# Kernel optimization log

Hardware: AMD Instinct MI355X
Metric: run time of the kernel (lower is better)

The kernel has to match this reference:

```python
import jax, jax.numpy as jnp
import numpy as np

B, D, S, L = 4, 512, 2048, 8921

def setup_inputs() -> dict:
    key = jax.random.key(0)
    ks = jax.random.split(key, 4)
    H = jax.random.normal(ks[0], (B, D, S), dtype=jnp.float32)
    # 1x1 conv weights collapse to [out, in] matrices (xavier-ish scale)
    Wk = jax.random.normal(ks[1], (D, D), dtype=jnp.float32) * (1.0 / np.sqrt(D))
    Wv = jax.random.normal(ks[2], (D, D), dtype=jnp.float32) * (1.0 / np.sqrt(D))
    bk = jnp.full((D,), 0.01, dtype=jnp.float32)
    bv = jnp.full((D,), 0.01, dtype=jnp.float32)
    Q = jax.random.normal(ks[3], (L, D), dtype=jnp.float32) * 0.02
    return {"H": H, "Wk": Wk, "bk": bk, "Wv": Wv, "bv": bv, "Q": Q}

def reference(H, Wk, bk, Wv, bv, Q):
    # K/V: 1x1 Conv1d over channels + bias, ELU, permute(0,2,1) -> [B,S,D]
    K = jax.nn.elu(jnp.einsum('od,bds->bso', Wk, H) + bk)
    V = jax.nn.elu(jnp.einsum('od,bds->bso', Wv, H) + bv)
    # TargetAttention: energy E = Q K^T -> [B,L,S], softmax over seq (scale=False)
    E = jnp.einsum('ld,bsd->bls', Q, K)
    A = jax.nn.softmax(E, axis=-1)
    C = jnp.einsum('bls,bsd->bld', A, V)  # [B, L, D]
    return (C, A)
```

## Files before the change

### kernel.cpp

```cpp
#include <hip/hip_runtime.h>
#include <math.h>

#define Bn 4
#define Dn 512
#define Sn 2048
#define Ln 8921
#define Lpad 8960

typedef short bf16x8 __attribute__((ext_vector_type(8)));
typedef float f32x4 __attribute__((ext_vector_type(4)));

__device__ __forceinline__ float elu1(float x) {
    return x > 0.f ? x : expm1f(x);
}

__device__ __forceinline__ unsigned f2bf(float f) {
    unsigned u = __float_as_uint(f);
    u += 0x7FFFu + ((u >> 16) & 1u);
    return u >> 16;
}
__device__ __forceinline__ unsigned pack2(float a, float b) {
    return f2bf(a) | (f2bf(b) << 16);
}
__device__ __forceinline__ unsigned pack_bf_trunc(float lo, float hi) {
    return __builtin_amdgcn_perm(__float_as_uint(hi), __float_as_uint(lo), 0x07060302u);
}
__device__ __forceinline__ void gld_lds16(const void* g, void* l) {
    __builtin_amdgcn_global_load_lds((const __attribute__((address_space(1))) int*)g,
                                     (__attribute__((address_space(3))) int*)l, 16, 0, 0);
}

__global__ __launch_bounds__(256) void h_transpose(const float* __restrict__ H,
                                                   short* __restrict__ Ht) {
    int b = blockIdx.z;
    int s0 = blockIdx.x * 64, d0 = blockIdx.y * 64;
    __shared__ float tile[64][65];
    int t = threadIdx.x;
    int r = t >> 4, c4 = (t & 15) * 4;
    const float* Hb = H + (size_t)b * Dn * Sn;
#pragma unroll
    for (int i = 0; i < 4; ++i) {
        float4 v = *(const float4*)(Hb + (size_t)(d0 + i * 16 + r) * Sn + s0 + c4);
        *(float4*)&tile[i * 16 + r][c4] = v;
    }
    __syncthreads();
#pragma unroll
    for (int i = 0; i < 4; ++i) {
        int srow = i * 16 + r;
        float v0 = tile[c4 + 0][srow], v1 = tile[c4 + 1][srow];
        float v2 = tile[c4 + 2][srow], v3 = tile[c4 + 3][srow];
        uint2 o = make_uint2(pack2(v0, v1), pack2(v2, v3));
        *(uint2*)(Ht + ((size_t)b * Sn + s0 + srow) * Dn + d0 + c4) = o;
    }
}

__global__ __launch_bounds__(256) void f32_to_bf16(const float* __restrict__ src,
                                                   short* __restrict__ dst, int n8) {
    int id = blockIdx.x * 256 + threadIdx.x;
    if (id >= n8) return;
    const float* s = src + (size_t)id * 8;
    float4 a = *(const float4*)s;
    float4 b = *(const float4*)(s + 4);
    uint4 o = {pack2(a.x, a.y), pack2(a.z, a.w), pack2(b.x, b.y), pack2(b.z, b.w)};
    *(uint4*)(dst + (size_t)id * 8) = o;
}

__global__ __launch_bounds__(256) void q_to_bf16(const float* __restrict__ Q,
                                                 short* __restrict__ Qb) {
    int id = blockIdx.x * 256 + threadIdx.x;
    int row = id >> 6, c = (id & 63) * 8;
    uint4 o = {0, 0, 0, 0};
    if (row < Ln) {
        const float* src = Q + (size_t)row * Dn + c;
        float4 a = *(const float4*)src;
        float4 b = *(const float4*)(src + 4);
        o.x = pack2(a.x, a.y); o.y = pack2(a.z, a.w);
        o.z = pack2(b.x, b.y); o.w = pack2(b.z, b.w);
    }
    *(uint4*)(Qb + (size_t)id * 8) = o;
}

template <int OUT_BF16, int EPI>
__global__ __launch_bounds__(256) void gemm_nt(const short* __restrict__ A,
                                               const short* __restrict__ B,
                                               const float* __restrict__ bias,
                                               void* __restrict__ Out,
                                               int K, int lda, int ldb, int ldo,
                                               int mmax,
                                               long bA, long bB, long bO) {
    const int b  = blockIdx.z;
    const int n0 = blockIdx.x * 128;
    const int m0 = blockIdx.y * 128;
    __shared__ short lA[128 * 32];
    __shared__ short lB[128 * 32];
    const int t = threadIdx.x;
    const int lane = t & 63, w = t >> 6;
    const int wm = (w & 1) * 64, wn = (w >> 1) * 64;
    const int quad = lane >> 4, l15 = lane & 15;
    f32x4 acc[4][4] = {};
    const short* Ab = A + (size_t)bA * b + (size_t)m0 * lda;
    const short* Bb = B + (size_t)bB * b + (size_t)n0 * ldb;
    const int sr = t >> 2, ss = (t & 3) * 8;

    for (int k0 = 0; k0 < K; k0 += 32) {
        gld_lds16(Ab + (size_t)sr * lda + k0 + ss,        lA + t * 8);
        gld_lds16(Ab + (size_t)(sr + 64) * lda + k0 + ss, lA + 2048 + t * 8);
        gld_lds16(Bb + (size_t)sr * ldb + k0 + ss,        lB + t * 8);
        gld_lds16(Bb + (size_t)(sr + 64) * ldb + k0 + ss, lB + 2048 + t * 8);
        __syncthreads();
        bf16x8 af[4], bfr[4];
#pragma unroll
        for (int i = 0; i < 4; ++i)
            af[i] = *(const bf16x8*)&lA[(wm + i * 16 + l15) * 32 + quad * 8];
#pragma unroll
        for (int j = 0; j < 4; ++j)
            bfr[j] = *(const bf16x8*)&lB[(wn + j * 16 + l15) * 32 + quad * 8];
#pragma unroll
        for (int i = 0; i < 4; ++i)
#pragma unroll
            for (int j = 0; j < 4; ++j)
                acc[i][j] = __builtin_amdgcn_mfma_f32_16x16x32_bf16(af[i], bfr[j], acc[i][j], 0, 0, 0);
        __syncthreads();
    }

#pragma unroll
    for (int i = 0; i < 4; ++i) {
        int mb = m0 + wm + i * 16 + quad * 4;
#pragma unroll
        for (int r = 0; r < 4; ++r) {
            int m = mb + r;
            if (m < mmax) {
                float bm = (EPI == 2) ? bias[m] : 0.f;
#pragma unroll
                for (int j = 0; j < 4; ++j) {
                    int col = n0 + wn + j * 16 + l15;
                    float v = acc[i][j][r];
                    if (EPI == 1) v = elu1(v + bias[col]);
                    if (EPI == 2) v = elu1(v + bm);
                    if (OUT_BF16)
                        ((short*)Out)[(size_t)bO * b + (size_t)m * ldo + col] = (short)f2bf(v);
                    else
                        ((float*)Out)[(size_t)bO * b + (size_t)m * ldo + col] = v;
                }
            }
        }
    }
}

template <int OUT_BF16>
__global__ __launch_bounds__(512, 2) void gemm_nt256(const short* __restrict__ A,
                                                     const short* __restrict__ B,
                                                     void* __restrict__ Out,
                                                     int K, int lda, int ldb, int ldo,
                                                     int mmax,
                                                     long bA, long bB, long bO) {
    const int b  = blockIdx.z;
    const int n0 = blockIdx.x * 256;
    const int m0 = blockIdx.y * 256;
    __shared__ short lds[65536];
    const int t = threadIdx.x;
    const int lane = t & 63, w = t >> 6;
    const int wm = w >> 2, wn = w & 3;
    const int quad = lane >> 4, l15 = lane & 15;
    const int xr = (l15 >> 1) & 3;

    const short* Ab = A + (size_t)bA * b + (size_t)m0 * lda;
    const short* Bb = B + (size_t)bB * b + (size_t)n0 * ldb;

    const short* srcA[2]; const short* srcB[2];
    int dstA[2], dstB[2];
#pragma unroll
    for (int i = 0; i < 2; ++i) {
        int p = i * 512 + t;
        int g = p ^ ((p >> 3) & 3);
        int row = g >> 2, q = g & 3;
        srcA[i] = Ab + (size_t)row * lda + q * 8;
        srcB[i] = Bb + (size_t)row * ldb + q * 8;
        dstA[i] = p * 8;
        dstB[i] = 8192 + p * 8;
    }

    int offA[8], offB[4];
#pragma unroll
    for (int m = 0; m < 8; ++m) {
        int c = (wm * 128 + m * 16 + l15) * 4 + quad;
        offA[m] = (c ^ xr) * 8;
    }
#pragma unroll
    for (int j = 0; j < 4; ++j) {
        int c = (wn * 64 + j * 16 + l15) * 4 + quad;
        offB[j] = 8192 + (c ^ xr) * 8;
    }

    f32x4 acc[8][4] = {};
    const int NK = K >> 5;

    auto STAGE = [&](int kt) {
        const int slot = (kt & 3) * 16384;
        const int ko = kt * 32;
#pragma unroll
        for (int i = 0; i < 2; ++i) {
            gld_lds16(srcA[i] + ko, &lds[slot + dstA[i]]);
            gld_lds16(srcB[i] + ko, &lds[slot + dstB[i]]);
        }
    };

    STAGE(0); STAGE(1); STAGE(2);

    for (int k = 0; k < NK; ++k) {
        asm volatile("s_waitcnt lgkmcnt(0)" ::: "memory");
        if (k < NK - 2)
            asm volatile("s_waitcnt vmcnt(8)" ::: "memory");
        else if (k == NK - 2)
            asm volatile("s_waitcnt vmcnt(4)" ::: "memory");
        else
            asm volatile("s_waitcnt vmcnt(0)" ::: "memory");
        __builtin_amdgcn_s_barrier();
        asm volatile("" ::: "memory");
        if (k + 3 < NK) STAGE(k + 3);
        const short* sl = &lds[(k & 3) * 16384];
        bf16x8 af[8], bfv[4];
#pragma unroll
        for (int m = 0; m < 8; ++m) af[m] = *(const bf16x8*)(sl + offA[m]);
#pragma unroll
        for (int j = 0; j < 4; ++j) bfv[j] = *(const bf16x8*)(sl + offB[j]);
#pragma unroll
        for (int m = 0; m < 8; ++m)
#pragma unroll
            for (int j = 0; j < 4; ++j)
                acc[m][j] = __builtin_amdgcn_mfma_f32_16x16x32_bf16(af[m], bfv[j], acc[m][j], 0, 0, 0);
    }

#pragma unroll
    for (int m = 0; m < 8; ++m) {
        int mb = m0 + wm * 128 + m * 16 + quad * 4;
#pragma unroll
        for (int r = 0; r < 4; ++r) {
            int mm = mb + r;
            if (mm < mmax) {
#pragma unroll
                for (int j = 0; j < 4; ++j) {
                    int col = n0 + wn * 64 + j * 16 + l15;
                    float v = acc[m][j][r];
                    if (OUT_BF16)
                        ((short*)Out)[(size_t)bO * b + (size_t)mm * ldo + col] = (short)f2bf(v);
                    else
                        ((float*)Out)[(size_t)bO * b + (size_t)mm * ldo + col] = v;
                }
            }
        }
    }
}

__global__ __launch_bounds__(256) void softmax_bf16(short* __restrict__ EA,
                                                    float* __restrict__ Aout) {
    int row = blockIdx.x;
    int b = row / Ln, l = row - b * Ln;
    short* pe = EA + ((size_t)b * Lpad + l) * Sn;
    float* pa = Aout + (size_t)row * Sn;
    int t = threadIdx.x;
    uint4 raw = *(const uint4*)(pe + t * 8);
    unsigned pw[4] = {raw.x, raw.y, raw.z, raw.w};
    float v[8];
#pragma unroll
    for (int q = 0; q < 4; ++q) {
        v[2 * q]     = __uint_as_float(pw[q] << 16);
        v[2 * q + 1] = __uint_as_float(pw[q] & 0xFFFF0000u);
    }
    float m = v[0];
#pragma unroll
    for (int i = 1; i < 8; ++i) m = fmaxf(m, v[i]);
#pragma unroll
    for (int off = 32; off >= 1; off >>= 1) m = fmaxf(m, __shfl_xor(m, off));
    __shared__ float sm[4], ssum[4];
    int lane = t & 63, wv = t >> 6;
    if (lane == 0) sm[wv] = m;
    __syncthreads();
    m = fmaxf(fmaxf(sm[0], sm[1]), fmaxf(sm[2], sm[3]));
    float s = 0.f;
#pragma unroll
    for (int i = 0; i < 8; ++i) {
        v[i] = expf(v[i] - m);
        s += v[i];
    }
#pragma unroll
    for (int off = 32; off >= 1; off >>= 1) s += __shfl_xor(s, off);
    if (lane == 0) ssum[wv] = s;
    __syncthreads();
    s = ssum[0] + ssum[1] + ssum[2] + ssum[3];
    float inv = 1.f / s;
#pragma unroll
    for (int i = 0; i < 8; ++i) v[i] *= inv;
    float4 o0 = {v[0], v[1], v[2], v[3]};
    float4 o1 = {v[4], v[5], v[6], v[7]};
    *(float4*)(pa + t * 8)     = o0;
    *(float4*)(pa + t * 8 + 4) = o1;
    uint4 ob = {pack2(v[0], v[1]), pack2(v[2], v[3]), pack2(v[4], v[5]), pack2(v[6], v[7])};
    *(uint4*)(pe + t * 8) = ob;
}

__global__ __launch_bounds__(256) void softmax_f32(float* __restrict__ E) {
    size_t row = blockIdx.x;
    float* p = E + row * (size_t)Sn;
    int t = threadIdx.x;
    float4 u0 = *(const float4*)(p + t * 8);
    float4 u1 = *(const float4*)(p + t * 8 + 4);
    float v[8] = {u0.x, u0.y, u0.z, u0.w, u1.x, u1.y, u1.z, u1.w};
    float m = v[0];
#pragma unroll
    for (int i = 1; i < 8; ++i) m = fmaxf(m, v[i]);
#pragma unroll
    for (int off = 32; off >= 1; off >>= 1) m = fmaxf(m, __shfl_xor(m, off));
    __shared__ float sm[4], ssum[4];
    int lane = t & 63, wv = t >> 6;
    if (lane == 0) sm[wv] = m;
    __syncthreads();
    m = fmaxf(fmaxf(sm[0], sm[1]), fmaxf(sm[2], sm[3]));
    float s = 0.f;
#pragma unroll
    for (int i = 0; i < 8; ++i) {
        v[i] = expf(v[i] - m);
        s += v[i];
    }
#pragma unroll
    for (int off = 32; off >= 1; off >>= 1) s += __shfl_xor(s, off);
    if (lane == 0) ssum[wv] = s;
    __syncthreads();
    s = ssum[0] + ssum[1] + ssum[2] + ssum[3];
    float inv = 1.f / s;
#pragma unroll
    for (int i = 0; i < 8; ++i) v[i] *= inv;
    float4 o0 = {v[0], v[1], v[2], v[3]};
    float4 o1 = {v[4], v[5], v[6], v[7]};
    *(float4*)(p + t * 8)     = o0;
    *(float4*)(p + t * 8 + 4) = o1;
}

__global__ __launch_bounds__(256) void c_mfma_f32(const float* __restrict__ A,
                                                  const short* __restrict__ Vt,
                                                  float* __restrict__ C) {
    const int b  = blockIdx.z;
    const int n0 = blockIdx.x * 128;
    const int m0 = blockIdx.y * 128;
    __shared__ short lA[128 * 32];
    __shared__ short lB[128 * 32];
    const int t = threadIdx.x;
    const int lane = t & 63, w = t >> 6;
    const int wm = (w & 1) * 64, wn = (w >> 1) * 64;
    const int quad = lane >> 4, l15 = lane & 15;
    f32x4 acc[4][4] = {};
    const float* Ab = A + (size_t)b * Ln * Sn;
    const short* Bb = Vt + (size_t)b * Dn * Sn + (size_t)n0 * Sn;
    const int ar = t >> 1, ah = (t & 1) * 16;
    const int br = t >> 2, bs = (t & 3) * 8;
    const int am = m0 + ar;
    const bool arow_ok = (am < Ln);
    const float* asrc0 = Ab + (size_t)am * Sn + ah;

    for (int s0 = 0; s0 < Sn; s0 += 32) {
        gld_lds16(Bb + (size_t)br * Sn + s0 + bs,        lB + t * 8);
        gld_lds16(Bb + (size_t)(br + 64) * Sn + s0 + bs, lB + 2048 + t * 8);
        unsigned p[8] = {0, 0, 0, 0, 0, 0, 0, 0};
        if (arow_ok) {
            const float* src = asrc0 + s0;
            float4 f0 = *(const float4*)(src);
            float4 f1 = *(const float4*)(src + 4);
            float4 f2 = *(const float4*)(src + 8);
            float4 f3 = *(const float4*)(src + 12);
            p[0] = pack_bf_trunc(f0.x, f0.y); p[1] = pack_bf_trunc(f0.z, f0.w);
            p[2] = pack_bf_trunc(f1.x, f1.y); p[3] = pack_bf_trunc(f1.z, f1.w);
            p[4] = pack_bf_trunc(f2.x, f2.y); p[5] = pack_bf_trunc(f2.z, f2.w);
            p[6] = pack_bf_trunc(f3.x, f3.y); p[7] = pack_bf_trunc(f3.z, f3.w);
        }
        *(uint4*)&lA[ar * 32 + ah]     = *(uint4*)&p[0];
        *(uint4*)&lA[ar * 32 + ah + 8] = *(uint4*)&p[4];
        __syncthreads();
        bf16x8 af[4], bfr[4];
#pragma unroll
        for (int i = 0; i < 4; ++i)
            af[i] = *(const bf16x8*)&lA[(wm + i * 16 + l15) * 32 + quad * 8];
#pragma unroll
        for (int j = 0; j < 4; ++j)
            bfr[j] = *(const bf16x8*)&lB[(wn + j * 16 + l15) * 32 + quad * 8];
#pragma unroll
        for (int i = 0; i < 4; ++i)
#pragma unroll
            for (int j = 0; j < 4; ++j)
                acc[i][j] = __builtin_amdgcn_mfma_f32_16x16x32_bf16(af[i], bfr[j], acc[i][j], 0, 0, 0);
        __syncthreads();
    }

#pragma unroll
    for (int i = 0; i < 4; ++i) {
        int mb = m0 + wm + i * 16 + quad * 4;
#pragma unroll
        for (int r = 0; r < 4; ++r) {
            int m = mb + r;
            if (m < Ln) {
                float* dst = C + (size_t)b * Ln * Dn + (size_t)m * Dn + n0 + wn;
#pragma unroll
                for (int j = 0; j < 4; ++j) dst[j * 16 + l15] = acc[i][j][r];
            }
        }
    }
}

extern "C" void kernel_launch(void* const* d_in, const int* in_sizes, int n_in,
                              void* d_out, int out_size, void* d_ws, size_t ws_size,
                              hipStream_t stream) {
    const float* H  = (const float*)d_in[0];
    const float* Wk = (const float*)d_in[1];
    const float* bk = (const float*)d_in[2];
    const float* Wv = (const float*)d_in[3];
    const float* bv = (const float*)d_in[4];
    const float* Q  = (const float*)d_in[5];

    float* out  = (float*)d_out;
    float* Cout = out;
    float* Aout = out + (size_t)Bn * Ln * Dn;

    short* Vt  = (short*)d_ws;
    short* Kb  = Vt + (size_t)Bn * Dn * Sn;
    short* Qb  = Kb + (size_t)Bn * Sn * Dn;
    short* EAb = Qb + (size_t)Lpad * Dn;
    short* Ht  = EAb;
    short* Wkb = Ht + (size_t)Bn * Sn * Dn;
    short* Wvb = Wkb + (size_t)Dn * Dn;

    size_t need_primary =
        2 * ((size_t)Bn * Dn * Sn + (size_t)Bn * Sn * Dn + (size_t)Lpad * Dn +
             (size_t)Bn * Lpad * Sn);
    bool big = ws_size >= need_primary;

    h_transpose<<<dim3(Sn / 64, Dn / 64, Bn), 256, 0, stream>>>(H, Ht);
    f32_to_bf16<<<(Dn * Dn / 8 + 255) / 256, 256, 0, stream>>>(Wk, Wkb, Dn * Dn / 8);
    f32_to_bf16<<<(Dn * Dn / 8 + 255) / 256, 256, 0, stream>>>(Wv, Wvb, Dn * Dn / 8);
    q_to_bf16<<<(Lpad * 64) / 256, 256, 0, stream>>>(Q, Qb);

    gemm_nt<1, 1><<<dim3(Dn / 128, Sn / 128, Bn), 256, 0, stream>>>(
        Ht, Wkb, bk, Kb, Dn, Dn, Dn, Dn, Sn,
        (long)Sn * Dn, 0L, (long)Sn * Dn);

    gemm_nt<1, 2><<<dim3(Sn / 128, Dn / 128, Bn), 256, 0, stream>>>(
        Wvb, Ht, bv, Vt, Dn, Dn, Dn, Sn, Dn,
        0L, (long)Sn * Dn, (long)Dn * Sn);

    if (big) {
        gemm_nt256<1><<<dim3(Sn / 256, Lpad / 256, Bn), 512, 0, stream>>>(
            Qb, Kb, EAb, Dn, Dn, Dn, Sn, Lpad,
            0L, (long)Sn * Dn, (long)Lpad * Sn);
        softmax_bf16<<<Bn * Ln, 256, 0, stream>>>(EAb, Aout);
        gemm_nt256<0><<<dim3(Dn / 256, Lpad / 256, Bn), 512, 0, stream>>>(
            EAb, Vt, Cout, Sn, Sn, Sn, Dn, Ln,
            (long)Lpad * Sn, (long)Dn * Sn, (long)Ln * Dn);
    } else {
        gemm_nt<0, 0><<<dim3(Sn / 128, Lpad / 128, Bn), 256, 0, stream>>>(
            Qb, Kb, nullptr, Aout, Dn, Dn, Dn, Sn, Ln,
            0L, (long)Sn * Dn, (long)Ln * Sn);
        softmax_f32<<<Bn * Ln, 256, 0, stream>>>(Aout);
        c_mfma_f32<<<dim3(Dn / 128, Lpad / 128, Bn), 256, 0, stream>>>(Aout, Vt, Cout);
    }
}
```

Measured before the change: 720.9 us.

## Split GEMM k-step into two phases, remap workgroups, use narrower tile for PV GEMM

The 256-wide NT GEMM becomes a template over the N tile width. The PV GEMM switches to a 256x128 tile, which doubles its workgroup count for better CU occupancy. Each k-iteration is split into two halves that interleave LDS fragment loads, global->LDS staging of A and B, and MFMA bursts wrapped in s_setprio. Workgroup IDs are also remapped across 8 groups, apparently to spread tiles across XCDs for cache locality. The extra barriers per iteration add synchronisation overhead, and the vmcnt counts must match the number of loads issued per stage.

```diff
diff --git a/kernel.cpp b/kernel.cpp
--- a/kernel.cpp
+++ b/kernel.cpp
@@ -147,43 +147,63 @@
     }
 }
 
-template <int OUT_BF16>
-__global__ __launch_bounds__(512, 2) void gemm_nt256(const short* __restrict__ A,
-                                                     const short* __restrict__ B,
-                                                     void* __restrict__ Out,
-                                                     int K, int lda, int ldb, int ldo,
-                                                     int mmax,
-                                                     long bA, long bB, long bO) {
-    const int b  = blockIdx.z;
-    const int n0 = blockIdx.x * 256;
-    const int m0 = blockIdx.y * 256;
-    __shared__ short lds[65536];
+template <int OUT_BF16, int BN>
+__global__ __launch_bounds__(512, 2) void gemm_ntp(const short* __restrict__ A,
+                                                   const short* __restrict__ B,
+                                                   void* __restrict__ Out,
+                                                   int K, int lda, int ldb, int ldo,
+                                                   int mmax,
+                                                   long bA, long bB, long bO) {
+    constexpr int NWN   = BN / 64;
+    constexpr int WSPAN = 32 * NWN;
+    constexpr int WMF   = 2 * NWN;
+    constexpr int BCH   = BN * 4;
+    constexpr int SLOT  = 8192 + BN * 32;
+    constexpr int TPB   = 2 + BN / 128;
+    __shared__ short lds[4 * SLOT];
+
+    int GX = gridDim.x, GY = gridDim.y;
+    int nwg = GX * GY * gridDim.z;
+    int lin = blockIdx.x + GX * (blockIdx.y + GY * blockIdx.z);
+    int wid = lin;
+    if ((nwg & 7) == 0) wid = (lin & 7) * (nwg >> 3) + (lin >> 3);
+    int bx = wid % GX; wid /= GX;
+    int by = wid % GY;
+    int bz = wid / GY;
+
+    const int b  = bz;
+    const int n0 = bx * BN;
+    const int m0 = by * 256;
     const int t = threadIdx.x;
     const int lane = t & 63, w = t >> 6;
-    const int wm = w >> 2, wn = w & 3;
+    const int wn = w % NWN, wm = w / NWN;
     const int quad = lane >> 4, l15 = lane & 15;
     const int xr = (l15 >> 1) & 3;
 
     const short* Ab = A + (size_t)bA * b + (size_t)m0 * lda;
     const short* Bb = B + (size_t)bB * b + (size_t)n0 * ldb;
 
-    const short* srcA[2]; const short* srcB[2];
-    int dstA[2], dstB[2];
+    const short* srcA[2]; int dstA[2];
 #pragma unroll
     for (int i = 0; i < 2; ++i) {
         int p = i * 512 + t;
         int g = p ^ ((p >> 3) & 3);
-        int row = g >> 2, q = g & 3;
-        srcA[i] = Ab + (size_t)row * lda + q * 8;
-        srcB[i] = Bb + (size_t)row * ldb + q * 8;
+        srcA[i] = Ab + (size_t)(g >> 2) * lda + (g & 3) * 8;
         dstA[i] = p * 8;
+    }
+    const short* srcB[2]; int dstB[2];
+#pragma unroll
+    for (int i = 0; i < BCH / 512; ++i) {
+        int p = i * 512 + t;
+        int g = p ^ ((p >> 3) & 3);
+        srcB[i] = Bb + (size_t)(g >> 2) * ldb + (g & 3) * 8;
         dstB[i] = 8192 + p * 8;
     }
 
-    int offA[8], offB[4];
-#pragma unroll
-    for (int m = 0; m < 8; ++m) {
-        int c = (wm * 128 + m * 16 + l15) * 4 + quad;
+    int offA[WMF], offB[4];
+#pragma unroll
+    for (int m = 0; m < WMF; ++m) {
+        int c = (wm * WSPAN + m * 16 + l15) * 4 + quad;
         offA[m] = (c ^ xr) * 8;
     }
 #pragma unroll
@@ -192,48 +212,75 @@
         offB[j] = 8192 + (c ^ xr) * 8;
     }
 
-    f32x4 acc[8][4] = {};
+    f32x4 acc[WMF][4] = {};
     const int NK = K >> 5;
 
-    auto STAGE = [&](int kt) {
-        const int slot = (kt & 3) * 16384;
+    auto STAGE_A = [&](int kt) {
+        const int slot = (kt & 3) * SLOT;
         const int ko = kt * 32;
-#pragma unroll
-        for (int i = 0; i < 2; ++i) {
-            gld_lds16(srcA[i] + ko, &lds[slot + dstA[i]]);
-            gld_lds16(srcB[i] + ko, &lds[slot + dstB[i]]);
-        }
+        gld_lds16(srcA[0] + ko, &lds[slot + dstA[0]]);
+        gld_lds16(srcA[1] + ko, &lds[slot + dstA[1]]);
     };
-
-    STAGE(0); STAGE(1); STAGE(2);
+    auto STAGE_B = [&](int kt) {
+        const int slot = (kt & 3) * SLOT;
+        const int ko = kt * 32;
+        gld_lds16(srcB[0] + ko, &lds[slot + dstB[0]]);
+        if constexpr (BN == 256) gld_lds16(srcB[1] + ko, &lds[slot + dstB[1]]);
+    };
+
+    STAGE_A(0); STAGE_B(0);
+    STAGE_A(1); STAGE_B(1);
+    STAGE_A(2); STAGE_B(2);
 
     for (int k = 0; k < NK; ++k) {
         asm volatile("s_waitcnt lgkmcnt(0)" ::: "memory");
-        if (k < NK - 2)
-            asm volatile("s_waitcnt vmcnt(8)" ::: "memory");
-        else if (k == NK - 2)
-            asm volatile("s_waitcnt vmcnt(4)" ::: "memory");
-        else
-            asm volatile("s_waitcnt vmcnt(0)" ::: "memory");
+        if constexpr (TPB == 4) {
+            if (k < NK - 2)       asm volatile("s_waitcnt vmcnt(8)" ::: "memory");
+            else if (k == NK - 2) asm volatile("s_waitcnt vmcnt(4)" ::: "memory");
+            else                  asm volatile("s_waitcnt vmcnt(0)" ::: "memory");
+        } else {
+            if (k < NK - 2)       asm volatile("s_waitcnt vmcnt(6)" ::: "memory");
+            else if (k == NK - 2) asm volatile("s_waitcnt vmcnt(3)" ::: "memory");
+            else                  asm volatile("s_waitcnt vmcnt(0)" ::: "memory");
+        }
         __builtin_amdgcn_s_barrier();
         asm volatile("" ::: "memory");
-        if (k + 3 < NK) STAGE(k + 3);
-        const short* sl = &lds[(k & 3) * 16384];
-        bf16x8 af[8], bfv[4];
-#pragma unroll
-        for (int m = 0; m < 8; ++m) af[m] = *(const bf16x8*)(sl + offA[m]);
+        const short* sl = &lds[(k & 3) * SLOT];
+
+        bf16x8 af[WMF], bfv[4];
 #pragma unroll
         for (int j = 0; j < 4; ++j) bfv[j] = *(const bf16x8*)(sl + offB[j]);
 #pragma unroll
-        for (int m = 0; m < 8; ++m)
+        for (int m = 0; m < WMF / 2; ++m) af[m] = *(const bf16x8*)(sl + offA[m]);
+        if (k + 3 < NK) STAGE_A(k + 3);
+        asm volatile("s_waitcnt lgkmcnt(0)" ::: "memory");
+        __builtin_amdgcn_s_barrier();
+        __builtin_amdgcn_s_setprio(1);
+#pragma unroll
+        for (int m = 0; m < WMF / 2; ++m)
 #pragma unroll
             for (int j = 0; j < 4; ++j)
                 acc[m][j] = __builtin_amdgcn_mfma_f32_16x16x32_bf16(af[m], bfv[j], acc[m][j], 0, 0, 0);
-    }
-
-#pragma unroll
-    for (int m = 0; m < 8; ++m) {
-        int mb = m0 + wm * 128 + m * 16 + quad * 4;
+        __builtin_amdgcn_s_setprio(0);
+        __builtin_amdgcn_s_barrier();
+
+#pragma unroll
+        for (int m = WMF / 2; m < WMF; ++m) af[m] = *(const bf16x8*)(sl + offA[m]);
+        if (k + 3 < NK) STAGE_B(k + 3);
+        asm volatile("s_waitcnt lgkmcnt(0)" ::: "memory");
+        __builtin_amdgcn_s_barrier();
+        __builtin_amdgcn_s_setprio(1);
+#pragma unroll
+        for (int m = WMF / 2; m < WMF; ++m)
+#pragma unroll
+            for (int j = 0; j < 4; ++j)
+                acc[m][j] = __builtin_amdgcn_mfma_f32_16x16x32_bf16(af[m], bfv[j], acc[m][j], 0, 0, 0);
+        __builtin_amdgcn_s_setprio(0);
+    }
+
+#pragma unroll
+    for (int m = 0; m < WMF; ++m) {
+        int mb = m0 + wm * WSPAN + m * 16 + quad * 4;
 #pragma unroll
         for (int r = 0; r < 4; ++r) {
             int mm = mb + r;
@@ -446,11 +493,11 @@
         0L, (long)Sn * Dn, (long)Dn * Sn);
 
     if (big) {
-        gemm_nt256<1><<<dim3(Sn / 256, Lpad / 256, Bn), 512, 0, stream>>>(
+        gemm_ntp<1, 256><<<dim3(Sn / 256, Lpad / 256, Bn), 512, 0, stream>>>(
             Qb, Kb, EAb, Dn, Dn, Dn, Sn, Lpad,
             0L, (long)Sn * Dn, (long)Lpad * Sn);
         softmax_bf16<<<Bn * Ln, 256, 0, stream>>>(EAb, Aout);
-        gemm_nt256<0><<<dim3(Dn / 256, Lpad / 256, Bn), 512, 0, stream>>>(
+        gemm_ntp<0, 128><<<dim3(Dn / 128, Lpad / 256, Bn), 512, 0, stream>>>(
             EAb, Vt, Cout, Sn, Sn, Sn, Dn, Ln,
             (long)Lpad * Sn, (long)Dn * Sn, (long)Ln * Dn);
     } else {
```

Result: no change. 724.6 us (+0.5%).
